# Kernel optimization log

Measured on AMD Instinct MI355X. Metric: run time of the kernel, lower is better.

Reference implementation:

```python
import jax, jax.numpy as jnp
import numpy as np

HIDDEN = 1024
INTER = 4096
NUM_EXPERTS = 8
TOP_K = 2


def setup_inputs() -> dict:
    key = jax.random.key(0)
    k1, k2, k3, k4 = jax.random.split(key, 4)
    hidden_states = jax.random.normal(k1, (4, 1024, HIDDEN), dtype=jnp.float32)
    gate_w = jax.random.normal(k2, (HIDDEN, NUM_EXPERTS), dtype=jnp.float32) * 0.02
    w1 = jax.random.normal(k3, (NUM_EXPERTS, HIDDEN, INTER), dtype=jnp.float32) * 0.02
    w2 = jax.random.normal(k4, (NUM_EXPERTS, INTER, HIDDEN), dtype=jnp.float32) * 0.02
    return {"hidden_states": hidden_states, "gate_w": gate_w, "w1": w1, "w2": w2}


def reference(hidden_states, gate_w, w1, w2):
    B, S, H = hidden_states.shape
    x = hidden_states.reshape(-1, H)                       # [T, H]
    T = x.shape[0]
    router_logits = x @ gate_w                             # [T, E]
    probs = jax.nn.softmax(router_logits.astype(jnp.float32), axis=-1)
    routing_weights, selected_experts = jax.lax.top_k(probs, TOP_K)  # [T, K]
    routing_weights = routing_weights / routing_weights.sum(-1, keepdims=True)
    routing_weights = routing_weights.astype(x.dtype)
    # combine[t, e] = sum_k rw[t, k] * (sel[t, k] == e)
    combine = jnp.zeros((T, NUM_EXPERTS), x.dtype).at[
        jnp.arange(T)[:, None], selected_experts
    ].add(routing_weights)
    # dense grouped MLP over all experts; zero combine weight drops unrouted pairs
    h1 = jax.nn.gelu(jnp.einsum('th,ehi->tei', x, w1), approximate=False)  # [T, E, I]
    y = jnp.einsum('tei,eih->teh', h1, w2)                 # [T, E, H]
    out = jnp.einsum('teh,te->th', y, combine)             # [T, H]
    return out.reshape(B, S, H), router_logits
```

## Files before the change

### kernel.cpp

```cpp
#include <hip/hip_runtime.h>
#include <hip/hip_bf16.h>
#include <math.h>

typedef unsigned short u16;
typedef unsigned int u32;
typedef __bf16 bf16x8 __attribute__((ext_vector_type(8)));
typedef float f32x4 __attribute__((ext_vector_type(4)));

#define T_TOK 4096
#define HID   1024
#define INTER 4096
#define NEXP  8

#define WS_NEEDED 209978368ull

__device__ __forceinline__ u16 bfc(float f) {
    return __builtin_bit_cast(u16, (__bf16)f);
}
__device__ __forceinline__ u32 pk2bf(float a, float b) {
    return (u32)__builtin_bit_cast(u16, (__bf16)a)
         | ((u32)__builtin_bit_cast(u16, (__bf16)b) << 16);
}

__device__ __forceinline__ void gl2lds16(const void* g, void* l) {
    __builtin_amdgcn_global_load_lds(
        (const __attribute__((address_space(1))) u32*)g,
        (__attribute__((address_space(3))) u32*)l, 16, 0, 0);
}

__device__ __forceinline__ float fast_gelu(float v) {
    float u2 = v * (-1.5957691216f - 0.0713548163f * v * v);
    return v / (1.0f + __expf(u2));
}

#define RTR_BLK 1024
#define TW_BLK  8192

__global__ __launch_bounds__(256) void preproc_kernel(
    const float* __restrict__ x, const float* __restrict__ gw,
    const float* __restrict__ w1, const float* __restrict__ w2,
    float* __restrict__ logits, int* __restrict__ counts,
    int* __restrict__ tlist, u32* __restrict__ sel, u16* __restrict__ xb,
    u16* __restrict__ w1t, u16* __restrict__ w2t)
{
    __shared__ float tl[64][65];
    const int bid = blockIdx.x;
    const int tid = threadIdx.x;

    if (bid < RTR_BLK) {
        const int lane = tid & 63, wv = tid >> 6;
        const int t = bid * 4 + wv;
        const float* xr = x + (size_t)t * HID;
        u16* xw = xb + (size_t)t * HID;
        float a[8] = {0.f,0.f,0.f,0.f,0.f,0.f,0.f,0.f};
        for (int h = lane; h < HID; h += 64) {
            float xv = xr[h];
            xw[h] = bfc(xv);
            const float4* g4 = (const float4*)(gw + h * 8);
            float4 g0 = g4[0], g1 = g4[1];
            a[0] += xv * g0.x; a[1] += xv * g0.y; a[2] += xv * g0.z; a[3] += xv * g0.w;
            a[4] += xv * g1.x; a[5] += xv * g1.y; a[6] += xv * g1.z; a[7] += xv * g1.w;
        }
#pragma unroll
        for (int e = 0; e < 8; e++) {
            float v = a[e];
            for (int o = 32; o > 0; o >>= 1) v += __shfl_down(v, o, 64);
            a[e] = v;
        }
        if (lane == 0) {
#pragma unroll
            for (int e = 0; e < 8; e++) logits[(size_t)t * 8 + e] = a[e];
            int e1 = 0; float b1 = a[0];
            for (int e = 1; e < 8; e++) if (a[e] > b1) { b1 = a[e]; e1 = e; }
            int e2 = -1; float b2 = -1e30f;
            for (int e = 0; e < 8; e++) if (e != e1 && a[e] > b2) { b2 = a[e]; e2 = e; }
            int p = atomicAdd(&counts[e1], 1);
            tlist[e1 * T_TOK + p] = t;
            sel[2 * t + 0] = (u32)e1 | ((u32)p << 3);
            p = atomicAdd(&counts[e2], 1);
            tlist[e2 * T_TOK + p] = t;
            sel[2 * t + 1] = (u32)e2 | ((u32)p << 3);
        }
        return;
    }

    const float* src; u16* dst; int R, C, id;
    if (bid < RTR_BLK + TW_BLK) { id = bid - RTR_BLK;          src = w1; dst = w1t; R = HID;   C = INTER; }
    else                        { id = bid - RTR_BLK - TW_BLK; src = w2; dst = w2t; R = INTER; C = HID;   }
    const int cpb = C >> 6, rpb = R >> 6;
    const int bx = id % cpb;
    const int tmp = id / cpb;
    const int by = tmp % rpb;
    const int e  = tmp / rpb;
    const int c0 = bx * 64, r0 = by * 64;
    const float* s = src + (size_t)e * R * C + (size_t)r0 * C + c0;
#pragma unroll
    for (int it = 0; it < 4; it++) {
        int idx = it * 256 + tid;
        int r = idx >> 4;
        int c4 = (idx & 15) * 4;
        float4 v = *(const float4*)(s + (size_t)r * C + c4);
        tl[c4 + 0][r] = v.x;
        tl[c4 + 1][r] = v.y;
        tl[c4 + 2][r] = v.z;
        tl[c4 + 3][r] = v.w;
    }
    __syncthreads();
    u16* d = dst + (size_t)e * C * R + (size_t)c0 * R + r0;
#pragma unroll
    for (int it = 0; it < 2; it++) {
        int idx = it * 256 + tid;
        int c = idx >> 3;
        int rg = (idx & 7) * 8;
        u32 o[4];
#pragma unroll
        for (int p = 0; p < 4; p++)
            o[p] = pk2bf(tl[c][rg + 2 * p], tl[c][rg + 2 * p + 1]);
        *(uint4*)(d + (size_t)c * R + rg) = *(uint4*)o;
    }
}

__global__ __launch_bounds__(256, 1) void gemm1_kernel(
    const u16* __restrict__ xb, const u16* __restrict__ w1t,
    const int* __restrict__ counts, const int* __restrict__ tlist,
    u16* __restrict__ h1b)
{
    const int e = blockIdx.z, mt = blockIdx.y, nt = blockIdx.x;
    const int cnt = counts[e];
    if (mt * 128 >= cnt) return;
    __shared__ __align__(16) u16 As[8192];
    __shared__ __align__(16) u16 Bs[8192];
    __shared__ int toks[128];
    const int tid = threadIdx.x, lane = tid & 63, wv = tid >> 6;
    if (tid < 128) toks[tid] = tlist[e * T_TOK + min(mt * 128 + tid, cnt - 1)];
    __syncthreads();

    f32x4 acc[4][4] = {};
    const int wm = wv & 1, wn = wv >> 1;
    const int sj = tid >> 3, sp = tid & 7;

    size_t abase[4], bbase[4];
    const u16* w1base = w1t + ((size_t)e * INTER + (size_t)nt * 128) * HID;
#pragma unroll
    for (int j = 0; j < 4; j++) {
        int m = j * 32 + sj;
        abase[j] = (size_t)toks[m] * HID + ((sp - m) & 7) * 8;
        bbase[j] = (size_t)m * HID + ((sp - m) & 7) * 8;
    }

    for (int h0 = 0; h0 < HID; h0 += 64) {
#pragma unroll
        for (int j = 0; j < 4; j++)
            gl2lds16(xb + abase[j] + h0, &As[j * 2048 + wv * 512]);
#pragma unroll
        for (int j = 0; j < 4; j++)
            gl2lds16(w1base + bbase[j] + h0, &Bs[j * 2048 + wv * 512]);
        __syncthreads();
#pragma unroll
        for (int kk = 0; kk < 2; kk++) {
            bf16x8 a[4], b[4];
            const int jjb = kk * 4 + (lane >> 4);
#pragma unroll
            for (int i = 0; i < 4; i++) {
                int m = wm * 64 + i * 16 + (lane & 15);
                a[i] = *(const bf16x8*)&As[m * 64 + ((jjb + m) & 7) * 8];
            }
#pragma unroll
            for (int i = 0; i < 4; i++) {
                int n = wn * 64 + i * 16 + (lane & 15);
                b[i] = *(const bf16x8*)&Bs[n * 64 + ((jjb + n) & 7) * 8];
            }
#pragma unroll
            for (int i = 0; i < 4; i++)
#pragma unroll
                for (int j = 0; j < 4; j++)
                    acc[i][j] = __builtin_amdgcn_mfma_f32_16x16x32_bf16(
                        a[i], b[j], acc[i][j], 0, 0, 0);
        }
        __syncthreads();
    }

    int prow = 0;
#pragma unroll
    for (int i = 0; i < 8; i++) prow += (i < e) ? counts[i] : 0;
    const int pb = prow + mt * 128;
    const bool full = (mt * 128 + 128 <= cnt);
#pragma unroll
    for (int i = 0; i < 4; i++) {
        const int mb = wm * 64 + i * 16 + ((lane >> 4) << 2);
#pragma unroll
        for (int j = 0; j < 4; j++) {
            const int n = nt * 128 + wn * 64 + j * 16 + (lane & 15);
#pragma unroll
            for (int r = 0; r < 4; r++) {
                const int m = mb + r;
                if (full || mt * 128 + m < cnt) {
                    h1b[(size_t)(pb + m) * INTER + n] = bfc(fast_gelu(acc[i][j][r]));
                }
            }
        }
    }
}

__global__ __launch_bounds__(256, 1) void gemm2_kernel(
    const u16* __restrict__ h1b, const u16* __restrict__ w2t,
    const int* __restrict__ counts, const int* __restrict__ tlist,
    float* __restrict__ y)
{
    const int e = blockIdx.z, mt = blockIdx.y;
    const int nt = blockIdx.x & 7, ks = blockIdx.x >> 3;
    const int cnt = counts[e];
    if (mt * 128 >= cnt) return;
    __shared__ __align__(16) u16 As[8192];
    __shared__ __align__(16) u16 Bs[8192];
    const int tid = threadIdx.x, lane = tid & 63, wv = tid >> 6;

    int prow = 0;
#pragma unroll
    for (int i = 0; i < 8; i++) prow += (i < e) ? counts[i] : 0;

    f32x4 acc[4][4] = {};
    const int wm = wv & 1, wn = wv >> 1;
    const int sj = tid >> 3, sp = tid & 7;

    size_t abase[4], bbase[4];
    const u16* w2base = w2t + ((size_t)e * HID + (size_t)nt * 128) * INTER;
#pragma unroll
    for (int j = 0; j < 4; j++) {
        int m = j * 32 + sj;
        int row = prow + min(mt * 128 + m, cnt - 1);
        abase[j] = (size_t)row * INTER + ((sp - m) & 7) * 8;
        bbase[j] = (size_t)m * INTER + ((sp - m) & 7) * 8;
    }

    const int i_lo = ks * (INTER / 2), i_hi = i_lo + (INTER / 2);
    for (int i0 = i_lo; i0 < i_hi; i0 += 64) {
#pragma unroll
        for (int j = 0; j < 4; j++)
            gl2lds16(h1b + abase[j] + i0, &As[j * 2048 + wv * 512]);
#pragma unroll
        for (int j = 0; j < 4; j++)
            gl2lds16(w2base + bbase[j] + i0, &Bs[j * 2048 + wv * 512]);
        __syncthreads();
#pragma unroll
        for (int kk = 0; kk < 2; kk++) {
            bf16x8 a[4], b[4];
            const int jjb = kk * 4 + (lane >> 4);
#pragma unroll
            for (int i = 0; i < 4; i++) {
                int m = wm * 64 + i * 16 + (lane & 15);
                a[i] = *(const bf16x8*)&As[m * 64 + ((jjb + m) & 7) * 8];
            }
#pragma unroll
            for (int i = 0; i < 4; i++) {
                int n = wn * 64 + i * 16 + (lane & 15);
                b[i] = *(const bf16x8*)&Bs[n * 64 + ((jjb + n) & 7) * 8];
            }
#pragma unroll
            for (int i = 0; i < 4; i++)
#pragma unroll
                for (int j = 0; j < 4; j++)
                    acc[i][j] = __builtin_amdgcn_mfma_f32_16x16x32_bf16(
                        a[i], b[j], acc[i][j], 0, 0, 0);
        }
        __syncthreads();
    }

    float* yk = y + (size_t)ks * (8192ull * HID);
    const bool full = (mt * 128 + 128 <= cnt);
#pragma unroll
    for (int i = 0; i < 4; i++) {
        const int mb = wm * 64 + i * 16 + ((lane >> 4) << 2);
#pragma unroll
        for (int j = 0; j < 4; j++) {
            const int n = nt * 128 + wn * 64 + j * 16 + (lane & 15);
#pragma unroll
            for (int r = 0; r < 4; r++) {
                const int m = mb + r;
                if (full || mt * 128 + m < cnt) {
                    yk[(size_t)(prow + mt * 128 + m) * HID + n] = acc[i][j][r];
                }
            }
        }
    }
}

__global__ __launch_bounds__(256) void combine_kernel(
    const float* __restrict__ y, const u32* __restrict__ sel,
    const int* __restrict__ counts, const float* __restrict__ logits,
    float* __restrict__ out)
{
    const int t = blockIdx.x;
    const u32 s0 = sel[2 * t + 0], s1 = sel[2 * t + 1];
    const int e0 = s0 & 7, p0 = s0 >> 3;
    const int e1 = s1 & 7, p1 = s1 >> 3;
    int off0 = 0, off1 = 0;
#pragma unroll
    for (int i = 0; i < 8; i++) {
        int c = counts[i];
        off0 += (i < e0) ? c : 0;
        off1 += (i < e1) ? c : 0;
    }
    const size_t g0 = (size_t)(off0 + p0) * HID;
    const size_t g1 = (size_t)(off1 + p1) * HID;
    const float la = logits[(size_t)t * 8 + e0];
    const float lb = logits[(size_t)t * 8 + e1];
    const float w0 = 1.0f / (1.0f + expf(lb - la));
    const float w1 = 1.0f - w0;

    const int c = threadIdx.x * 4;
    const float* y1p = y + 8192ull * HID;
    f32x4 a0 = *(const f32x4*)(y + g0 + c);
    f32x4 a1 = *(const f32x4*)(y1p + g0 + c);
    f32x4 b0 = *(const f32x4*)(y + g1 + c);
    f32x4 b1 = *(const f32x4*)(y1p + g1 + c);
    f32x4 o = w0 * (a0 + a1) + w1 * (b0 + b1);
    *(f32x4*)(out + (size_t)t * HID + c) = o;
}

extern "C" void kernel_launch(void* const* d_in, const int* in_sizes, int n_in,
                              void* d_out, int out_size, void* d_ws, size_t ws_size,
                              hipStream_t stream)
{
    const float* x  = (const float*)d_in[0];
    const float* gw = (const float*)d_in[1];
    const float* w1 = (const float*)d_in[2];
    const float* w2 = (const float*)d_in[3];
    float* out    = (float*)d_out;
    float* logits = out + 4194304;

    char* ws = (char*)d_ws;
    int*   counts = (int*)ws;
    int*   tlist  = (int*)(ws + 1024);
    u32*   sel    = (u32*)(ws + 132096);
    u16*   xb     = (u16*)(ws + 263168);
    u16*   w1t    = (u16*)(ws + 8651776);
    float* y      = (float*)(ws + 8651776);
    u16*   w2t    = (u16*)(ws + 75760640);
    u16*   h1b    = (u16*)(ws + 142869504);

    if (ws_size < WS_NEEDED) return;

    hipMemsetAsync(counts, 0, 256, stream);

    preproc_kernel<<<RTR_BLK + 2 * TW_BLK, 256, 0, stream>>>(
        x, gw, w1, w2, logits, counts, tlist, sel, xb, w1t, w2t);

    gemm1_kernel<<<dim3(32, 16, 8), 256, 0, stream>>>(xb, w1t, counts, tlist, h1b);
    gemm2_kernel<<<dim3(16, 16, 8), 256, 0, stream>>>(h1b, w2t, counts, tlist, y);
    combine_kernel<<<T_TOK, 256, 0, stream>>>(y, sel, counts, logits, out);
}
```

Measured before the change: 664.8 us.

## Pre-tile expert weights into LDS-image blocks and remap gemm2 grid

```diff
diff --git a/kernel.cpp b/kernel.cpp
--- a/kernel.cpp
+++ b/kernel.cpp
@@ -41,7 +41,7 @@
     const float* __restrict__ w1, const float* __restrict__ w2,
     float* __restrict__ logits, int* __restrict__ counts,
     int* __restrict__ tlist, u32* __restrict__ sel, u16* __restrict__ xb,
-    u16* __restrict__ w1t, u16* __restrict__ w2t)
+    u16* __restrict__ w1s, u16* __restrict__ w2s)
 {
     __shared__ float tl[64][65];
     const int bid = blockIdx.x;
@@ -85,8 +85,8 @@
     }
 
     const float* src; u16* dst; int R, C, id;
-    if (bid < RTR_BLK + TW_BLK) { id = bid - RTR_BLK;          src = w1; dst = w1t; R = HID;   C = INTER; }
-    else                        { id = bid - RTR_BLK - TW_BLK; src = w2; dst = w2t; R = INTER; C = HID;   }
+    if (bid < RTR_BLK + TW_BLK) { id = bid - RTR_BLK;          src = w1; dst = w1s; R = HID;   C = INTER; }
+    else                        { id = bid - RTR_BLK - TW_BLK; src = w2; dst = w2s; R = INTER; C = HID;   }
     const int cpb = C >> 6, rpb = R >> 6;
     const int bx = id % cpb;
     const int tmp = id / cpb;
@@ -106,22 +106,26 @@
         tl[c4 + 3][r] = v.w;
     }
     __syncthreads();
-    u16* d = dst + (size_t)e * C * R + (size_t)c0 * R + r0;
+    const int mbase = ((c0 >> 6) & 1) << 6;
+    u16* img = dst + (((size_t)e * (C >> 7) + (size_t)(c0 >> 7)) * (size_t)(R >> 6) + by) * 8192
+                   + (size_t)mbase * 64;
 #pragma unroll
     for (int it = 0; it < 2; it++) {
         int idx = it * 256 + tid;
         int c = idx >> 3;
-        int rg = (idx & 7) * 8;
+        int sp = idx & 7;
+        int m = mbase + c;
+        int rg = ((sp - m) & 7) * 8;
         u32 o[4];
 #pragma unroll
         for (int p = 0; p < 4; p++)
             o[p] = pk2bf(tl[c][rg + 2 * p], tl[c][rg + 2 * p + 1]);
-        *(uint4*)(d + (size_t)c * R + rg) = *(uint4*)o;
+        *(uint4*)(img + (size_t)c * 64 + sp * 8) = *(uint4*)o;
     }
 }
 
 __global__ __launch_bounds__(256, 1) void gemm1_kernel(
-    const u16* __restrict__ xb, const u16* __restrict__ w1t,
+    const u16* __restrict__ xb, const u16* __restrict__ w1s,
     const int* __restrict__ counts, const int* __restrict__ tlist,
     u16* __restrict__ h1b)
 {
@@ -139,14 +143,13 @@
     const int wm = wv & 1, wn = wv >> 1;
     const int sj = tid >> 3, sp = tid & 7;
 
-    size_t abase[4], bbase[4];
-    const u16* w1base = w1t + ((size_t)e * INTER + (size_t)nt * 128) * HID;
+    size_t abase[4];
 #pragma unroll
     for (int j = 0; j < 4; j++) {
         int m = j * 32 + sj;
         abase[j] = (size_t)toks[m] * HID + ((sp - m) & 7) * 8;
-        bbase[j] = (size_t)m * HID + ((sp - m) & 7) * 8;
-    }
+    }
+    const u16* img1 = w1s + (size_t)(e * 32 + nt) * 16 * 8192 + (size_t)tid * 8;
 
     for (int h0 = 0; h0 < HID; h0 += 64) {
 #pragma unroll
@@ -154,7 +157,7 @@
             gl2lds16(xb + abase[j] + h0, &As[j * 2048 + wv * 512]);
 #pragma unroll
         for (int j = 0; j < 4; j++)
-            gl2lds16(w1base + bbase[j] + h0, &Bs[j * 2048 + wv * 512]);
+            gl2lds16(img1 + ((size_t)h0 << 7) + j * 2048, &Bs[j * 2048 + wv * 512]);
         __syncthreads();
 #pragma unroll
         for (int kk = 0; kk < 2; kk++) {
@@ -203,12 +206,18 @@
 }
 
 __global__ __launch_bounds__(256, 1) void gemm2_kernel(
-    const u16* __restrict__ h1b, const u16* __restrict__ w2t,
+    const u16* __restrict__ h1b, const u16* __restrict__ w2s,
     const int* __restrict__ counts, const int* __restrict__ tlist,
     float* __restrict__ y)
 {
-    const int e = blockIdx.z, mt = blockIdx.y;
-    const int nt = blockIdx.x & 7, ks = blockIdx.x >> 3;
+    const int id = blockIdx.x;
+    const int gl = id & 7;
+    const int rest = id >> 3;
+    const int q  = rest & 15;
+    const int gx = rest >> 4;
+    const int g  = gx * 8 + gl;
+    const int e  = g >> 4, mt = g & 15;
+    const int nt = q & 7, ks = q >> 3;
     const int cnt = counts[e];
     if (mt * 128 >= cnt) return;
     __shared__ __align__(16) u16 As[8192];
@@ -223,15 +232,14 @@
     const int wm = wv & 1, wn = wv >> 1;
     const int sj = tid >> 3, sp = tid & 7;
 
-    size_t abase[4], bbase[4];
-    const u16* w2base = w2t + ((size_t)e * HID + (size_t)nt * 128) * INTER;
+    size_t abase[4];
 #pragma unroll
     for (int j = 0; j < 4; j++) {
         int m = j * 32 + sj;
         int row = prow + min(mt * 128 + m, cnt - 1);
         abase[j] = (size_t)row * INTER + ((sp - m) & 7) * 8;
-        bbase[j] = (size_t)m * INTER + ((sp - m) & 7) * 8;
-    }
+    }
+    const u16* img2 = w2s + (size_t)(e * 8 + nt) * 64 * 8192 + (size_t)tid * 8;
 
     const int i_lo = ks * (INTER / 2), i_hi = i_lo + (INTER / 2);
     for (int i0 = i_lo; i0 < i_hi; i0 += 64) {
@@ -240,7 +248,7 @@
             gl2lds16(h1b + abase[j] + i0, &As[j * 2048 + wv * 512]);
 #pragma unroll
         for (int j = 0; j < 4; j++)
-            gl2lds16(w2base + bbase[j] + i0, &Bs[j * 2048 + wv * 512]);
+            gl2lds16(img2 + ((size_t)i0 << 7) + j * 2048, &Bs[j * 2048 + wv * 512]);
         __syncthreads();
 #pragma unroll
         for (int kk = 0; kk < 2; kk++) {
@@ -334,9 +342,9 @@
     int*   tlist  = (int*)(ws + 1024);
     u32*   sel    = (u32*)(ws + 132096);
     u16*   xb     = (u16*)(ws + 263168);
-    u16*   w1t    = (u16*)(ws + 8651776);
+    u16*   w1s    = (u16*)(ws + 8651776);
     float* y      = (float*)(ws + 8651776);
-    u16*   w2t    = (u16*)(ws + 75760640);
+    u16*   w2s    = (u16*)(ws + 75760640);
     u16*   h1b    = (u16*)(ws + 142869504);
 
     if (ws_size < WS_NEEDED) return;
@@ -344,9 +352,9 @@
     hipMemsetAsync(counts, 0, 256, stream);
 
     preproc_kernel<<<RTR_BLK + 2 * TW_BLK, 256, 0, stream>>>(
-        x, gw, w1, w2, logits, counts, tlist, sel, xb, w1t, w2t);
-
-    gemm1_kernel<<<dim3(32, 16, 8), 256, 0, stream>>>(xb, w1t, counts, tlist, h1b);
-    gemm2_kernel<<<dim3(16, 16, 8), 256, 0, stream>>>(h1b, w2t, counts, tlist, y);
+        x, gw, w1, w2, logits, counts, tlist, sel, xb, w1s, w2s);
+
+    gemm1_kernel<<<dim3(32, 16, 8), 256, 0, stream>>>(xb, w1s, counts, tlist, h1b);
+    gemm2_kernel<<<2048, 256, 0, stream>>>(h1b, w2s, counts, tlist, y);
     combine_kernel<<<T_TOK, 256, 0, stream>>>(y, sel, counts, logits, out);
 }
```

Result: faster. 632.7 us (-4.8%).
